# Kernel tuning notes

Measured on AMD Instinct MI355X. Metric: run time of the kernel, lower is better.

Reference implementation:

```python
import jax, jax.numpy as jnp
import numpy as np

B, D, LC, LQ = 64, 128, 1024, 128
NEG = -1e30


def setup_inputs() -> dict:
    key = jax.random.key(0)
    k1, k2, k3 = jax.random.split(key, 3)
    lim = float(np.sqrt(1.0 / D))
    return {
        "C": jax.random.normal(k1, (B, D, LC), dtype=jnp.float32),
        "Q": jax.random.normal(k2, (B, D, LQ), dtype=jnp.float32),
        "cmask": jnp.ones((B, LC), dtype=jnp.float32),
        "qmask": jnp.ones((B, LQ), dtype=jnp.float32),
        "w": jax.random.uniform(k3, (3 * D,), dtype=jnp.float32, minval=-lim, maxval=lim),
    }


def reference(C, Q, cmask, qmask, w):
    # C: [B, D, Lc], Q: [B, D, Lq] -> transpose to [B, L, D] as in the torch module
    Ct = jnp.swapaxes(C, 1, 2)  # [B, Lc, D]
    Qt = jnp.swapaxes(Q, 1, 2)  # [B, Lq, D]
    d = Ct.shape[-1]
    # Trilinear decomposition of the per-step concat([Qi, C, Q*C]) . w loop:
    # S[b,c,q] = Qt[b,q] . w_q + Ct[b,c] . w_c + (Ct[b,c] * w_m) . Qt[b,q]
    w_q, w_c, w_m = w[:d], w[d:2 * d], w[2 * d:]
    s_q = Qt @ w_q                                   # [B, Lq]
    s_c = Ct @ w_c                                   # [B, Lc]
    s_m = jnp.einsum("bcd,bqd->bcq", Ct * w_m, Qt)   # [B, Lc, Lq]
    S = s_m + s_c[:, :, None] + s_q[:, None, :]      # [B, Lc, Lq]

    S1 = jax.nn.softmax(S + (1.0 - qmask)[:, None, :] * NEG, axis=2)
    S2 = jax.nn.softmax(S + (1.0 - cmask)[:, :, None] * NEG, axis=1)

    A = jnp.einsum("bcq,bqd->bcd", S1, Qt)           # [B, Lc, D]
    S12 = jnp.einsum("bcq,bkq->bck", S1, S2)         # [B, Lc, Lc]
    Bt = jnp.einsum("bck,bkd->bcd", S12, Ct)         # [B, Lc, D]

    out = jnp.concatenate([Ct, A, Ct * A, Ct * Bt], axis=2)  # [B, Lc, 4D]
    # dropout is identity in eval mode
    return jnp.swapaxes(out, 1, 2)                   # [B, 4D, Lc]
```

## Files before the change

kernel.cpp:

```cpp
#include <hip/hip_runtime.h>
#include <cstdint>
#include <cstddef>

#define B_  64
#define D_  128
#define LC_ 1024
#define LQ_ 128
#define NEGV (-1e30f)
#define NINF (-3.402823466e38f)

typedef short s16x8 __attribute__((ext_vector_type(8)));
typedef float f32x4 __attribute__((ext_vector_type(4)));

__device__ __forceinline__ unsigned short f2bf(float x) {
    union { float f; unsigned u; } v; v.f = x;
    unsigned r = v.u + 0x7fffu + ((v.u >> 16) & 1u);
    return (unsigned short)(r >> 16);
}

__global__ __launch_bounds__(256) void kT_C(const float* __restrict__ C,
                                            const float* __restrict__ w,
                                            unsigned short* __restrict__ CWt) {
    __shared__ float tile[32][33];
    int t = threadIdx.x;
    int c0 = blockIdx.x * 32, d0 = blockIdx.y * 32, b = blockIdx.z;
    int cc = t & 31, r8 = t >> 5;
#pragma unroll
    for (int i = 0; i < 4; i++) {
        int dd = r8 + 8 * i;
        tile[dd][cc] = C[((size_t)b * D_ + d0 + dd) * LC_ + c0 + cc] * w[2 * D_ + d0 + dd];
    }
    __syncthreads();
#pragma unroll
    for (int i = 0; i < 4; i++) {
        int c2 = r8 + 8 * i;
        CWt[((size_t)b * LC_ + c0 + c2) * D_ + d0 + cc] = f2bf(tile[cc][c2]);
    }
}

__global__ __launch_bounds__(256) void kT_Q(const float* __restrict__ Q,
                                            unsigned short* __restrict__ Qt) {
    __shared__ float tile[32][33];
    int t = threadIdx.x;
    int q0 = blockIdx.x * 32, d0 = blockIdx.y * 32, b = blockIdx.z;
    int qq = t & 31, r8 = t >> 5;
#pragma unroll
    for (int i = 0; i < 4; i++) {
        int dd = r8 + 8 * i;
        tile[dd][qq] = Q[((size_t)b * D_ + d0 + dd) * LQ_ + q0 + qq];
    }
    __syncthreads();
#pragma unroll
    for (int i = 0; i < 4; i++) {
        int q2 = r8 + 8 * i;
        Qt[((size_t)b * LQ_ + q0 + q2) * D_ + d0 + qq] = f2bf(tile[qq][q2]);
    }
}

__global__ __launch_bounds__(256) void k0_sq(const float* __restrict__ Q,
                                             const float* __restrict__ w,
                                             float* __restrict__ sq_g) {
    int idx = blockIdx.x * 256 + threadIdx.x;
    int b = idx >> 7, q = idx & 127;
    float s = 0.f;
    for (int d = 0; d < D_; d++) s += Q[((size_t)b * D_ + d) * LQ_ + q] * w[d];
    sq_g[idx] = s;
}

__global__ __launch_bounds__(256) void k0_sc(const float* __restrict__ C,
                                             const float* __restrict__ w,
                                             float* __restrict__ sc_g) {
    int idx = blockIdx.x * 256 + threadIdx.x;
    int b = idx >> 10, c = idx & 1023;
    float s = 0.f;
    for (int d = 0; d < D_; d++) s += C[((size_t)b * D_ + d) * LC_ + c] * w[D_ + d];
    sc_g[idx] = s;
}

__global__ __launch_bounds__(256) void kA_S(const unsigned short* __restrict__ CWt,
                                            const unsigned short* __restrict__ Qt,
                                            const float* __restrict__ sc_g,
                                            const float* __restrict__ sq_g,
                                            float* __restrict__ S_g) {
    __shared__ unsigned short Aw[128 * 136];
    __shared__ unsigned short Bq[128 * 136];
    __shared__ float sc_l[128], sq_l[128];
    int t = threadIdx.x;
    int b = blockIdx.y, c0 = blockIdx.x * 128;
    if (t < 128) {
        sc_l[t] = sc_g[b * LC_ + c0 + t];
        sq_l[t] = sq_g[b * LQ_ + t];
    }
    const uint4* gA = (const uint4*)(CWt + ((size_t)b * LC_ + c0) * D_);
    const uint4* gB = (const uint4*)(Qt + (size_t)b * LQ_ * D_);
#pragma unroll
    for (int i = 0; i < 8; i++) {
        int g = i * 256 + t;
        int row = g >> 4, col = g & 15;
        *(uint4*)&Aw[row * 136 + col * 8] = gA[g];
        *(uint4*)&Bq[row * 136 + col * 8] = gB[g];
    }
    __syncthreads();
    int w = t >> 6, l = t & 63, quad = l >> 4, lp = l & 15;
    int w32 = w * 32;
    f32x4 zero = {0.f, 0.f, 0.f, 0.f};
    f32x4 acc[2][8];
#pragma unroll
    for (int mc = 0; mc < 2; mc++)
#pragma unroll
        for (int qt = 0; qt < 8; qt++) acc[mc][qt] = zero;

#pragma unroll
    for (int ks = 0; ks < 4; ks++) {
        s16x8 a[2], bb[8];
        a[0] = *(const s16x8*)&Aw[(w32 + lp) * 136 + ks * 32 + quad * 8];
        a[1] = *(const s16x8*)&Aw[(w32 + 16 + lp) * 136 + ks * 32 + quad * 8];
#pragma unroll
        for (int qt = 0; qt < 8; qt++)
            bb[qt] = *(const s16x8*)&Bq[(qt * 16 + lp) * 136 + ks * 32 + quad * 8];
#pragma unroll
        for (int mc = 0; mc < 2; mc++)
#pragma unroll
            for (int qt = 0; qt < 8; qt++)
                acc[mc][qt] = __builtin_amdgcn_mfma_f32_16x16x32_bf16(a[mc], bb[qt], acc[mc][qt], 0, 0, 0);
    }
#pragma unroll
    for (int mc = 0; mc < 2; mc++)
#pragma unroll
        for (int i = 0; i < 4; i++) {
            int cl = w32 + mc * 16 + quad * 4 + i;
            float scv = sc_l[cl];
            size_t rb = ((size_t)b * LC_ + c0 + cl) * LQ_;
#pragma unroll
            for (int qt = 0; qt < 8; qt++) {
                int q = qt * 16 + lp;
                S_g[rb + q] = acc[mc][qt][i] + scv + sq_l[q];
            }
        }
}

__global__ __launch_bounds__(256) void krow(const float* __restrict__ S_g,
                                            const float* __restrict__ qmask,
                                            float* __restrict__ rowmax_g,
                                            float* __restrict__ rowsum_g) {
    int t = threadIdx.x, w = t >> 6, l = t & 63;
    int b = blockIdx.y;
    int r = blockIdx.x * 4 + w;
    size_t rb = ((size_t)b * LC_ + r) * LQ_;
    float v0 = S_g[rb + l] + (1.0f - qmask[b * LQ_ + l]) * NEGV;
    float v1 = S_g[rb + 64 + l] + (1.0f - qmask[b * LQ_ + 64 + l]) * NEGV;
    float m = fmaxf(v0, v1);
#pragma unroll
    for (int off = 1; off < 64; off <<= 1) m = fmaxf(m, __shfl_xor(m, off, 64));
    float s = __expf(v0 - m) + __expf(v1 - m);
#pragma unroll
    for (int off = 1; off < 64; off <<= 1) s += __shfl_xor(s, off, 64);
    if (l == 0) { rowmax_g[b * LC_ + r] = m; rowsum_g[b * LC_ + r] = s; }
}

__global__ __launch_bounds__(128) void k2a(const float* __restrict__ S_g,
                                           const float* __restrict__ cmask,
                                           float* __restrict__ pmax,
                                           float* __restrict__ psum) {
    int q = threadIdx.x;
    int b = blockIdx.y;
    int chunk = blockIdx.x;
    int cbase = chunk * 32;
    float m = NINF, s = 0.f;
    for (int cc = 0; cc < 32; cc++) {
        int c = cbase + cc;
        float v = S_g[((size_t)b * LC_ + c) * LQ_ + q] + (1.0f - cmask[b * LC_ + c]) * NEGV;
        float mn = fmaxf(m, v);
        s = s * __expf(m - mn) + __expf(v - mn);
        m = mn;
    }
    pmax[((size_t)b * 32 + chunk) * LQ_ + q] = m;
    psum[((size_t)b * 32 + chunk) * LQ_ + q] = s;
}

__global__ __launch_bounds__(128) void k2b(const float* __restrict__ pmax,
                                           const float* __restrict__ psum,
                                           float* __restrict__ colmax_g,
                                           float* __restrict__ colsum_g) {
    int q = threadIdx.x;
    int b = blockIdx.x;
    float m = NINF;
    for (int j = 0; j < 32; j++) m = fmaxf(m, pmax[((size_t)b * 32 + j) * LQ_ + q]);
    float s = 0.f;
    for (int j = 0; j < 32; j++)
        s += psum[((size_t)b * 32 + j) * LQ_ + q] * __expf(pmax[((size_t)b * 32 + j) * LQ_ + q] - m);
    colmax_g[b * LQ_ + q] = m;
    colsum_g[b * LQ_ + q] = s;
}

__global__ __launch_bounds__(256) void kB_T2(const float* __restrict__ C,
                                             const float* __restrict__ S_g,
                                             const float* __restrict__ cmask,
                                             const float* __restrict__ colmax_g,
                                             float* __restrict__ T2p) {
    __shared__ unsigned short Ca[128 * 40];
    __shared__ unsigned short Et[128 * 40];
    __shared__ float cm_l[128];
    int t = threadIdx.x;
    int b = blockIdx.y, kc = blockIdx.x;
    int cbase = kc * 256;
    if (t < 128) cm_l[t] = colmax_g[b * LQ_ + t];
    int w = t >> 6, l = t & 63, quad = l >> 4, lp = l & 15;
    int w32 = w * 32;
    f32x4 zero = {0.f, 0.f, 0.f, 0.f};
    f32x4 acc[2][8];
#pragma unroll
    for (int mc = 0; mc < 2; mc++)
#pragma unroll
        for (int qt = 0; qt < 8; qt++) acc[mc][qt] = zero;
    __syncthreads();

    for (int cb = 0; cb < 256; cb += 32) {
        {
            int d = t >> 1, half = t & 1;
            const float4* src = (const float4*)(C + ((size_t)b * D_ + d) * LC_ + cbase + cb + half * 16);
            unsigned short* dst = &Ca[d * 40 + half * 16];
#pragma unroll
            for (int j = 0; j < 4; j++) {
                float4 v = src[j];
                ushort4 o;
                o.x = f2bf(v.x); o.y = f2bf(v.y); o.z = f2bf(v.z); o.w = f2bf(v.w);
                *(ushort4*)&dst[j * 4] = o;
            }
        }
        {
            int cc = t >> 3, qb = (t & 7) * 16;
            int cg = cbase + cb + cc;
            float cmv = (1.0f - cmask[b * LC_ + cg]) * NEGV;
            const float4* src = (const float4*)(S_g + ((size_t)b * LC_ + cg) * LQ_ + qb);
#pragma unroll
            for (int j = 0; j < 4; j++) {
                float4 v = src[j];
                int q = qb + j * 4;
                Et[(q + 0) * 40 + cc] = f2bf(__expf(v.x + cmv - cm_l[q + 0]));
                Et[(q + 1) * 40 + cc] = f2bf(__expf(v.y + cmv - cm_l[q + 1]));
                Et[(q + 2) * 40 + cc] = f2bf(__expf(v.z + cmv - cm_l[q + 2]));
                Et[(q + 3) * 40 + cc] = f2bf(__expf(v.w + cmv - cm_l[q + 3]));
            }
        }
        __syncthreads();
        s16x8 a[2], bb[8];
        a[0] = *(const s16x8*)&Ca[(w32 + lp) * 40 + quad * 8];
        a[1] = *(const s16x8*)&Ca[(w32 + 16 + lp) * 40 + quad * 8];
#pragma unroll
        for (int qt = 0; qt < 8; qt++)
            bb[qt] = *(const s16x8*)&Et[(qt * 16 + lp) * 40 + quad * 8];
#pragma unroll
        for (int mc = 0; mc < 2; mc++)
#pragma unroll
            for (int qt = 0; qt < 8; qt++)
                acc[mc][qt] = __builtin_amdgcn_mfma_f32_16x16x32_bf16(a[mc], bb[qt], acc[mc][qt], 0, 0, 0);
        __syncthreads();
    }
    size_t base = (size_t)kc * ((size_t)B_ * D_ * LQ_) + (size_t)b * D_ * LQ_;
#pragma unroll
    for (int mc = 0; mc < 2; mc++)
#pragma unroll
        for (int i = 0; i < 4; i++) {
            int d = w32 + mc * 16 + quad * 4 + i;
#pragma unroll
            for (int qt = 0; qt < 8; qt++)
                T2p[base + (size_t)d * LQ_ + qt * 16 + lp] = acc[mc][qt][i];
        }
}

__global__ __launch_bounds__(256) void k3b(const float* __restrict__ T2p,
                                           const float* __restrict__ colsum_g,
                                           float* __restrict__ T2s) {
    int idx = blockIdx.x * 256 + threadIdx.x;
    const int N = B_ * D_ * LQ_;
    int b = idx >> 14, q = idx & 127;
    float s = T2p[idx] + T2p[idx + N] + T2p[idx + 2 * N] + T2p[idx + 3 * N];
    T2s[idx] = s / colsum_g[b * LQ_ + q];
}

__global__ __launch_bounds__(256) void kC_out(const float* __restrict__ C,
                                              const float* __restrict__ Q,
                                              const float* __restrict__ qmask,
                                              const float* __restrict__ S_g,
                                              const float* __restrict__ rowmax_g,
                                              const float* __restrict__ rowsum_g,
                                              const float* __restrict__ T2s,
                                              float* __restrict__ out) {
    __shared__ unsigned short S1[128 * 136];
    __shared__ unsigned short Aq[128 * 72];
    __shared__ unsigned short At[128 * 72];
    __shared__ float rm_l[128], ri_l[128], qm_l[128];
    int t = threadIdx.x;
    int b = blockIdx.y, c0 = blockIdx.x * 128;
    if (t < 128) {
        rm_l[t] = rowmax_g[b * LC_ + c0 + t];
        ri_l[t] = 1.0f / rowsum_g[b * LC_ + c0 + t];
        qm_l[t] = qmask[b * LQ_ + t];
    }
    __syncthreads();
    {
        int cc = t >> 1, qb = (t & 1) * 64;
        float rm = rm_l[cc], ri = ri_l[cc];
        const float4* src = (const float4*)(S_g + ((size_t)b * LC_ + c0 + cc) * LQ_ + qb);
        unsigned short* dst = &S1[cc * 136 + qb];
#pragma unroll
        for (int j = 0; j < 16; j++) {
            float4 v = src[j];
            int q = qb + j * 4;
            ushort4 o;
            o.x = f2bf(__expf(v.x + (1.0f - qm_l[q + 0]) * NEGV - rm) * ri);
            o.y = f2bf(__expf(v.y + (1.0f - qm_l[q + 1]) * NEGV - rm) * ri);
            o.z = f2bf(__expf(v.z + (1.0f - qm_l[q + 2]) * NEGV - rm) * ri);
            o.w = f2bf(__expf(v.w + (1.0f - qm_l[q + 3]) * NEGV - rm) * ri);
            *(ushort4*)&dst[j * 4] = o;
        }
    }
    int w = t >> 6, l = t & 63, quad = l >> 4, lp = l & 15;
    int w32 = w * 32;
    f32x4 zero = {0.f, 0.f, 0.f, 0.f};
    f32x4 accA[2][8], accB[2][8];
#pragma unroll
    for (int mc = 0; mc < 2; mc++)
#pragma unroll
        for (int nt = 0; nt < 8; nt++) { accA[mc][nt] = zero; accB[mc][nt] = zero; }

    for (int kq = 0; kq < 2; kq++) {
        __syncthreads();
        {
            int d = t >> 1, qoff = (t & 1) * 32;
            const float4* sq4 = (const float4*)(Q + ((size_t)b * D_ + d) * LQ_ + kq * 64 + qoff);
            const float4* st4 = (const float4*)(T2s + ((size_t)b * D_ + d) * LQ_ + kq * 64 + qoff);
            unsigned short* dq = &Aq[d * 72 + qoff];
            unsigned short* dt = &At[d * 72 + qoff];
#pragma unroll
            for (int j = 0; j < 8; j++) {
                float4 v = sq4[j];
                ushort4 o;
                o.x = f2bf(v.x); o.y = f2bf(v.y); o.z = f2bf(v.z); o.w = f2bf(v.w);
                *(ushort4*)&dq[j * 4] = o;
                float4 u = st4[j];
                ushort4 p;
                p.x = f2bf(u.x); p.y = f2bf(u.y); p.z = f2bf(u.z); p.w = f2bf(u.w);
                *(ushort4*)&dt[j * 4] = p;
            }
        }
        __syncthreads();
#pragma unroll
        for (int ks = 0; ks < 2; ks++) {
            s16x8 aq[2], at[2], bb[8];
            aq[0] = *(const s16x8*)&Aq[(w32 + lp) * 72 + ks * 32 + quad * 8];
            aq[1] = *(const s16x8*)&Aq[(w32 + 16 + lp) * 72 + ks * 32 + quad * 8];
            at[0] = *(const s16x8*)&At[(w32 + lp) * 72 + ks * 32 + quad * 8];
            at[1] = *(const s16x8*)&At[(w32 + 16 + lp) * 72 + ks * 32 + quad * 8];
#pragma unroll
            for (int nt = 0; nt < 8; nt++)
                bb[nt] = *(const s16x8*)&S1[(nt * 16 + lp) * 136 + kq * 64 + ks * 32 + quad * 8];
#pragma unroll
            for (int mc = 0; mc < 2; mc++)
#pragma unroll
                for (int nt = 0; nt < 8; nt++) {
                    accA[mc][nt] = __builtin_amdgcn_mfma_f32_16x16x32_bf16(aq[mc], bb[nt], accA[mc][nt], 0, 0, 0);
                    accB[mc][nt] = __builtin_amdgcn_mfma_f32_16x16x32_bf16(at[mc], bb[nt], accB[mc][nt], 0, 0, 0);
                }
        }
    }
    const size_t DL = (size_t)D_ * LC_;
#pragma unroll
    for (int mc = 0; mc < 2; mc++)
#pragma unroll
        for (int i = 0; i < 4; i++) {
            int d = w32 + mc * 16 + quad * 4 + i;
            const float* Crow = C + ((size_t)b * D_ + d) * LC_ + c0;
            size_t ob = ((size_t)b * 4 * D_ + d) * LC_ + c0;
#pragma unroll
            for (int nt = 0; nt < 8; nt++) {
                int c = nt * 16 + lp;
                float cv = Crow[c];
                float a = accA[mc][nt][i];
                float bt = accB[mc][nt][i];
                out[ob + c] = cv;
                out[ob + DL + c] = a;
                out[ob + 2 * DL + c] = cv * a;
                out[ob + 3 * DL + c] = cv * bt;
            }
        }
}

extern "C" void kernel_launch(void* const* d_in, const int* in_sizes, int n_in,
                              void* d_out, int out_size, void* d_ws, size_t ws_size,
                              hipStream_t stream) {
    const float* C     = (const float*)d_in[0];
    const float* Q     = (const float*)d_in[1];
    const float* cmask = (const float*)d_in[2];
    const float* qmask = (const float*)d_in[3];
    const float* w     = (const float*)d_in[4];
    float* out = (float*)d_out;

    float* ws = (float*)d_ws;
    float* S_g      = ws;
    float* rowmax_g = S_g + (size_t)B_ * LC_ * LQ_;
    float* rowsum_g = rowmax_g + (size_t)B_ * LC_;
    float* pmax     = rowsum_g + (size_t)B_ * LC_;
    float* psum     = pmax + (size_t)B_ * 32 * LQ_;
    float* colmax_g = psum + (size_t)B_ * 32 * LQ_;
    float* colsum_g = colmax_g + (size_t)B_ * LQ_;
    float* sq_g     = colsum_g + (size_t)B_ * LQ_;
    float* sc_g     = sq_g + (size_t)B_ * LQ_;
    float* T2p      = sc_g + (size_t)B_ * LC_;
    float* T2s      = T2p + (size_t)4 * B_ * D_ * LQ_;
    unsigned short* CWt = (unsigned short*)(T2s + (size_t)B_ * D_ * LQ_);
    unsigned short* Qt  = CWt + (size_t)B_ * LC_ * D_;

    kT_C<<<dim3(LC_ / 32, D_ / 32, B_), 256, 0, stream>>>(C, w, CWt);
    kT_Q<<<dim3(LQ_ / 32, D_ / 32, B_), 256, 0, stream>>>(Q, Qt);
    k0_sq<<<dim3(B_ * LQ_ / 256), 256, 0, stream>>>(Q, w, sq_g);
    k0_sc<<<dim3(B_ * LC_ / 256), 256, 0, stream>>>(C, w, sc_g);
    kA_S<<<dim3(LC_ / 128, B_), 256, 0, stream>>>(CWt, Qt, sc_g, sq_g, S_g);
    krow<<<dim3(LC_ / 4, B_), 256, 0, stream>>>(S_g, qmask, rowmax_g, rowsum_g);
    k2a<<<dim3(32, B_), 128, 0, stream>>>(S_g, cmask, pmax, psum);
    k2b<<<dim3(B_), 128, 0, stream>>>(pmax, psum, colmax_g, colsum_g);
    kB_T2<<<dim3(4, B_), 256, 0, stream>>>(C, S_g, cmask, colmax_g, T2p);
    k3b<<<dim3(B_ * D_ * LQ_ / 256), 256, 0, stream>>>(T2p, colsum_g, T2s);
    kC_out<<<dim3(LC_ / 128, B_), 256, 0, stream>>>(C, Q, qmask, S_g, rowmax_g,
                                                    rowsum_g, T2s, out);
}
```

Baseline: 265.8 us.

## Fuse softmax statistics into score GEMM and store bf16 probabilities instead of fp32 scores

The score kernel now computes the row softmax and the per-chunk column max and sum in registers. It writes bf16 S1 probabilities and a per-row factor instead of the full fp32 S matrix. The transpose kernels also produce the s_c/s_q dot products and bf16 copies of C and Q, so the separate reduction kernels and repeated fp32-to-bf16 conversions go away. The main cost removed is the fp32 S round trip through global memory and several extra launches. S2 is rebuilt algebraically from S1 with row and column scale factors, which risks overflow or precision loss because it relies on exp of large maxima, and the MFMA operands are now read straight from global memory without LDS staging.

```diff
diff --git a/kernel.cpp b/kernel.cpp
--- a/kernel.cpp
+++ b/kernel.cpp
@@ -17,92 +17,140 @@
     unsigned r = v.u + 0x7fffu + ((v.u >> 16) & 1u);
     return (unsigned short)(r >> 16);
 }
+__device__ __forceinline__ float bf2f(unsigned short x) {
+    union { unsigned u; float f; } v; v.u = ((unsigned)x) << 16;
+    return v.f;
+}
 
 __global__ __launch_bounds__(256) void kT_C(const float* __restrict__ C,
                                             const float* __restrict__ w,
-                                            unsigned short* __restrict__ CWt) {
+                                            unsigned short* __restrict__ CWt,
+                                            unsigned short* __restrict__ Cb,
+                                            float* __restrict__ sc_g) {
     __shared__ float tile[32][33];
+    __shared__ float wc_l[128], wm_l[128];
+    __shared__ float red[8][32];
     int t = threadIdx.x;
-    int c0 = blockIdx.x * 32, d0 = blockIdx.y * 32, b = blockIdx.z;
-    int cc = t & 31, r8 = t >> 5;
-#pragma unroll
-    for (int i = 0; i < 4; i++) {
-        int dd = r8 + 8 * i;
-        tile[dd][cc] = C[((size_t)b * D_ + d0 + dd) * LC_ + c0 + cc] * w[2 * D_ + d0 + dd];
-    }
-    __syncthreads();
-#pragma unroll
-    for (int i = 0; i < 4; i++) {
-        int c2 = r8 + 8 * i;
-        CWt[((size_t)b * LC_ + c0 + c2) * D_ + d0 + cc] = f2bf(tile[cc][c2]);
+    int b = blockIdx.y, c0 = blockIdx.x * 32;
+    if (t < 128) { wc_l[t] = w[D_ + t]; wm_l[t] = w[2 * D_ + t]; }
+    __syncthreads();
+    float scp = 0.f;
+    int cc = t & 31, db = t >> 5;
+    for (int ch = 0; ch < 4; ch++) {
+#pragma unroll
+        for (int i = 0; i < 4; i++) {
+            int dl = db * 4 + i;
+            float v = C[((size_t)(b * D_ + ch * 32 + dl)) * LC_ + c0 + cc];
+            tile[dl][cc] = v;
+            scp += v * wc_l[ch * 32 + dl];
+        }
+        __syncthreads();
+        {
+            int c2 = t >> 3, ds = (t & 7) * 4;
+            ushort4 o;
+            o.x = f2bf(tile[ds + 0][c2] * wm_l[ch * 32 + ds + 0]);
+            o.y = f2bf(tile[ds + 1][c2] * wm_l[ch * 32 + ds + 1]);
+            o.z = f2bf(tile[ds + 2][c2] * wm_l[ch * 32 + ds + 2]);
+            o.w = f2bf(tile[ds + 3][c2] * wm_l[ch * 32 + ds + 3]);
+            *(ushort4*)&CWt[((size_t)(b * LC_ + c0 + c2)) * D_ + ch * 32 + ds] = o;
+        }
+        {
+            int d2 = t >> 3, cs = (t & 7) * 4;
+            ushort4 o;
+            o.x = f2bf(tile[d2][cs + 0]);
+            o.y = f2bf(tile[d2][cs + 1]);
+            o.z = f2bf(tile[d2][cs + 2]);
+            o.w = f2bf(tile[d2][cs + 3]);
+            *(ushort4*)&Cb[((size_t)(b * D_ + ch * 32 + d2)) * LC_ + c0 + cs] = o;
+        }
+        __syncthreads();
+    }
+    red[db][cc] = scp;
+    __syncthreads();
+    if (t < 32) {
+        float s = 0.f;
+#pragma unroll
+        for (int j = 0; j < 8; j++) s += red[j][t];
+        sc_g[b * LC_ + c0 + t] = s;
     }
 }
 
 __global__ __launch_bounds__(256) void kT_Q(const float* __restrict__ Q,
-                                            unsigned short* __restrict__ Qt) {
+                                            const float* __restrict__ w,
+                                            unsigned short* __restrict__ Qt,
+                                            unsigned short* __restrict__ Qb,
+                                            float* __restrict__ sq_g) {
     __shared__ float tile[32][33];
+    __shared__ float wq_l[128];
+    __shared__ float red[8][32];
     int t = threadIdx.x;
-    int q0 = blockIdx.x * 32, d0 = blockIdx.y * 32, b = blockIdx.z;
-    int qq = t & 31, r8 = t >> 5;
-#pragma unroll
-    for (int i = 0; i < 4; i++) {
-        int dd = r8 + 8 * i;
-        tile[dd][qq] = Q[((size_t)b * D_ + d0 + dd) * LQ_ + q0 + qq];
-    }
-    __syncthreads();
-#pragma unroll
-    for (int i = 0; i < 4; i++) {
-        int q2 = r8 + 8 * i;
-        Qt[((size_t)b * LQ_ + q0 + q2) * D_ + d0 + qq] = f2bf(tile[qq][q2]);
-    }
-}
-
-__global__ __launch_bounds__(256) void k0_sq(const float* __restrict__ Q,
-                                             const float* __restrict__ w,
-                                             float* __restrict__ sq_g) {
-    int idx = blockIdx.x * 256 + threadIdx.x;
-    int b = idx >> 7, q = idx & 127;
-    float s = 0.f;
-    for (int d = 0; d < D_; d++) s += Q[((size_t)b * D_ + d) * LQ_ + q] * w[d];
-    sq_g[idx] = s;
-}
-
-__global__ __launch_bounds__(256) void k0_sc(const float* __restrict__ C,
-                                             const float* __restrict__ w,
-                                             float* __restrict__ sc_g) {
-    int idx = blockIdx.x * 256 + threadIdx.x;
-    int b = idx >> 10, c = idx & 1023;
-    float s = 0.f;
-    for (int d = 0; d < D_; d++) s += C[((size_t)b * D_ + d) * LC_ + c] * w[D_ + d];
-    sc_g[idx] = s;
+    int b = blockIdx.y, q0 = blockIdx.x * 32;
+    if (t < 128) wq_l[t] = w[t];
+    __syncthreads();
+    float sqp = 0.f;
+    int qq = t & 31, db = t >> 5;
+    for (int ch = 0; ch < 4; ch++) {
+#pragma unroll
+        for (int i = 0; i < 4; i++) {
+            int dl = db * 4 + i;
+            float v = Q[((size_t)(b * D_ + ch * 32 + dl)) * LQ_ + q0 + qq];
+            tile[dl][qq] = v;
+            sqp += v * wq_l[ch * 32 + dl];
+        }
+        __syncthreads();
+        {
+            int q2 = t >> 3, ds = (t & 7) * 4;
+            ushort4 o;
+            o.x = f2bf(tile[ds + 0][q2]);
+            o.y = f2bf(tile[ds + 1][q2]);
+            o.z = f2bf(tile[ds + 2][q2]);
+            o.w = f2bf(tile[ds + 3][q2]);
+            *(ushort4*)&Qt[((size_t)(b * LQ_ + q0 + q2)) * D_ + ch * 32 + ds] = o;
+        }
+        {
+            int d2 = t >> 3, qs = (t & 7) * 4;
+            ushort4 o;
+            o.x = f2bf(tile[d2][qs + 0]);
+            o.y = f2bf(tile[d2][qs + 1]);
+            o.z = f2bf(tile[d2][qs + 2]);
+            o.w = f2bf(tile[d2][qs + 3]);
+            *(ushort4*)&Qb[((size_t)(b * D_ + ch * 32 + d2)) * LQ_ + q0 + qs] = o;
+        }
+        __syncthreads();
+    }
+    red[db][qq] = sqp;
+    __syncthreads();
+    if (t < 32) {
+        float s = 0.f;
+#pragma unroll
+        for (int j = 0; j < 8; j++) s += red[j][t];
+        sq_g[b * LQ_ + q0 + t] = s;
+    }
 }
 
 __global__ __launch_bounds__(256) void kA_S(const unsigned short* __restrict__ CWt,
                                             const unsigned short* __restrict__ Qt,
                                             const float* __restrict__ sc_g,
                                             const float* __restrict__ sq_g,
-                                            float* __restrict__ S_g) {
-    __shared__ unsigned short Aw[128 * 136];
-    __shared__ unsigned short Bq[128 * 136];
-    __shared__ float sc_l[128], sq_l[128];
+                                            const float* __restrict__ cmask,
+                                            const float* __restrict__ qmask,
+                                            unsigned short* __restrict__ S1b,
+                                            float* __restrict__ g_g,
+                                            float* __restrict__ pmax_g,
+                                            float* __restrict__ psum_g) {
+    __shared__ unsigned short S1t[128 * 136];
+    __shared__ float sc_l[128], sq_l[128], cmv_l[128], qmv_l[128];
     int t = threadIdx.x;
     int b = blockIdx.y, c0 = blockIdx.x * 128;
     if (t < 128) {
         sc_l[t] = sc_g[b * LC_ + c0 + t];
         sq_l[t] = sq_g[b * LQ_ + t];
-    }
-    const uint4* gA = (const uint4*)(CWt + ((size_t)b * LC_ + c0) * D_);
-    const uint4* gB = (const uint4*)(Qt + (size_t)b * LQ_ * D_);
-#pragma unroll
-    for (int i = 0; i < 8; i++) {
-        int g = i * 256 + t;
-        int row = g >> 4, col = g & 15;
-        *(uint4*)&Aw[row * 136 + col * 8] = gA[g];
-        *(uint4*)&Bq[row * 136 + col * 8] = gB[g];
-    }
-    __syncthreads();
-    int w = t >> 6, l = t & 63, quad = l >> 4, lp = l & 15;
-    int w32 = w * 32;
+        cmv_l[t] = (1.0f - cmask[b * LC_ + c0 + t]) * NEGV;
+        qmv_l[t] = (1.0f - qmask[b * LQ_ + t]) * NEGV;
+    }
+    __syncthreads();
+    int wv = t >> 6, l = t & 63, quad = l >> 4, lp = l & 15;
+    int w32 = wv * 32;
     f32x4 zero = {0.f, 0.f, 0.f, 0.f};
     f32x4 acc[2][8];
 #pragma unroll
@@ -113,11 +161,11 @@
 #pragma unroll
     for (int ks = 0; ks < 4; ks++) {
         s16x8 a[2], bb[8];
-        a[0] = *(const s16x8*)&Aw[(w32 + lp) * 136 + ks * 32 + quad * 8];
-        a[1] = *(const s16x8*)&Aw[(w32 + 16 + lp) * 136 + ks * 32 + quad * 8];
+        a[0] = *(const s16x8*)&CWt[((size_t)(b * LC_ + c0 + w32 + lp)) * D_ + ks * 32 + quad * 8];
+        a[1] = *(const s16x8*)&CWt[((size_t)(b * LC_ + c0 + w32 + 16 + lp)) * D_ + ks * 32 + quad * 8];
 #pragma unroll
         for (int qt = 0; qt < 8; qt++)
-            bb[qt] = *(const s16x8*)&Bq[(qt * 16 + lp) * 136 + ks * 32 + quad * 8];
+            bb[qt] = *(const s16x8*)&Qt[((size_t)(b * LQ_ + qt * 16 + lp)) * D_ + ks * 32 + quad * 8];
 #pragma unroll
         for (int mc = 0; mc < 2; mc++)
 #pragma unroll
@@ -127,197 +175,180 @@
 #pragma unroll
     for (int mc = 0; mc < 2; mc++)
 #pragma unroll
+        for (int qt = 0; qt < 8; qt++)
+#pragma unroll
+            for (int i = 0; i < 4; i++)
+                acc[mc][qt][i] += sc_l[w32 + mc * 16 + quad * 4 + i] + sq_l[qt * 16 + lp];
+
+    float qmv_r[8];
+#pragma unroll
+    for (int qt = 0; qt < 8; qt++) qmv_r[qt] = qmv_l[qt * 16 + lp];
+
+    float rm_r[2][4], ri_r[2][4];
+#pragma unroll
+    for (int mc = 0; mc < 2; mc++)
+#pragma unroll
         for (int i = 0; i < 4; i++) {
-            int cl = w32 + mc * 16 + quad * 4 + i;
-            float scv = sc_l[cl];
-            size_t rb = ((size_t)b * LC_ + c0 + cl) * LQ_;
-#pragma unroll
-            for (int qt = 0; qt < 8; qt++) {
-                int q = qt * 16 + lp;
-                S_g[rb + q] = acc[mc][qt][i] + scv + sq_l[q];
+            float m = NINF;
+#pragma unroll
+            for (int qt = 0; qt < 8; qt++) m = fmaxf(m, acc[mc][qt][i] + qmv_r[qt]);
+#pragma unroll
+            for (int off = 1; off < 16; off <<= 1) m = fmaxf(m, __shfl_xor(m, off, 64));
+            float s = 0.f;
+#pragma unroll
+            for (int qt = 0; qt < 8; qt++) s += __expf(acc[mc][qt][i] + qmv_r[qt] - m);
+#pragma unroll
+            for (int off = 1; off < 16; off <<= 1) s += __shfl_xor(s, off, 64);
+            rm_r[mc][i] = m;
+            ri_r[mc][i] = 1.0f / s;
+            int row = w32 + mc * 16 + quad * 4 + i;
+            if (lp == 0) g_g[b * LC_ + c0 + row] = s * __expf(m + cmv_l[row]);
+        }
+
+    float cmv_r[2][4];
+#pragma unroll
+    for (int mc = 0; mc < 2; mc++)
+#pragma unroll
+        for (int i = 0; i < 4; i++) cmv_r[mc][i] = cmv_l[w32 + mc * 16 + quad * 4 + i];
+    int chunk = blockIdx.x * 4 + wv;
+#pragma unroll
+    for (int qt = 0; qt < 8; qt++) {
+        float cm = NINF;
+#pragma unroll
+        for (int mc = 0; mc < 2; mc++)
+#pragma unroll
+            for (int i = 0; i < 4; i++) cm = fmaxf(cm, acc[mc][qt][i] + cmv_r[mc][i]);
+        cm = fmaxf(cm, __shfl_xor(cm, 16, 64));
+        cm = fmaxf(cm, __shfl_xor(cm, 32, 64));
+        float cs = 0.f;
+#pragma unroll
+        for (int mc = 0; mc < 2; mc++)
+#pragma unroll
+            for (int i = 0; i < 4; i++) cs += __expf(acc[mc][qt][i] + cmv_r[mc][i] - cm);
+        cs += __shfl_xor(cs, 16, 64);
+        cs += __shfl_xor(cs, 32, 64);
+        if (l < 16) {
+            pmax_g[((size_t)(b * 32 + chunk)) * LQ_ + qt * 16 + lp] = cm;
+            psum_g[((size_t)(b * 32 + chunk)) * LQ_ + qt * 16 + lp] = cs;
+        }
+    }
+
+#pragma unroll
+    for (int mc = 0; mc < 2; mc++)
+#pragma unroll
+        for (int qt = 0; qt < 8; qt++)
+#pragma unroll
+            for (int i = 0; i < 4; i++) {
+                int row = w32 + mc * 16 + quad * 4 + i;
+                float s1 = __expf(acc[mc][qt][i] + qmv_r[qt] - rm_r[mc][i]) * ri_r[mc][i];
+                S1t[row * 136 + qt * 16 + lp] = f2bf(s1);
             }
-        }
-}
-
-__global__ __launch_bounds__(256) void krow(const float* __restrict__ S_g,
-                                            const float* __restrict__ qmask,
-                                            float* __restrict__ rowmax_g,
-                                            float* __restrict__ rowsum_g) {
-    int t = threadIdx.x, w = t >> 6, l = t & 63;
-    int b = blockIdx.y;
-    int r = blockIdx.x * 4 + w;
-    size_t rb = ((size_t)b * LC_ + r) * LQ_;
-    float v0 = S_g[rb + l] + (1.0f - qmask[b * LQ_ + l]) * NEGV;
-    float v1 = S_g[rb + 64 + l] + (1.0f - qmask[b * LQ_ + 64 + l]) * NEGV;
-    float m = fmaxf(v0, v1);
-#pragma unroll
-    for (int off = 1; off < 64; off <<= 1) m = fmaxf(m, __shfl_xor(m, off, 64));
-    float s = __expf(v0 - m) + __expf(v1 - m);
-#pragma unroll
-    for (int off = 1; off < 64; off <<= 1) s += __shfl_xor(s, off, 64);
-    if (l == 0) { rowmax_g[b * LC_ + r] = m; rowsum_g[b * LC_ + r] = s; }
-}
-
-__global__ __launch_bounds__(128) void k2a(const float* __restrict__ S_g,
-                                           const float* __restrict__ cmask,
-                                           float* __restrict__ pmax,
-                                           float* __restrict__ psum) {
-    int q = threadIdx.x;
-    int b = blockIdx.y;
-    int chunk = blockIdx.x;
-    int cbase = chunk * 32;
-    float m = NINF, s = 0.f;
-    for (int cc = 0; cc < 32; cc++) {
-        int c = cbase + cc;
-        float v = S_g[((size_t)b * LC_ + c) * LQ_ + q] + (1.0f - cmask[b * LC_ + c]) * NEGV;
-        float mn = fmaxf(m, v);
-        s = s * __expf(m - mn) + __expf(v - mn);
-        m = mn;
-    }
-    pmax[((size_t)b * 32 + chunk) * LQ_ + q] = m;
-    psum[((size_t)b * 32 + chunk) * LQ_ + q] = s;
+    __syncthreads();
+    {
+        int row = t >> 1, qh = (t & 1) * 64;
+        const uint4* src = (const uint4*)&S1t[row * 136 + qh];
+        uint4* dst = (uint4*)&S1b[((size_t)(b * LC_ + c0 + row)) * LQ_ + qh];
+#pragma unroll
+        for (int j = 0; j < 8; j++) dst[j] = src[j];
+    }
 }
 
 __global__ __launch_bounds__(128) void k2b(const float* __restrict__ pmax,
                                            const float* __restrict__ psum,
-                                           float* __restrict__ colmax_g,
-                                           float* __restrict__ colsum_g) {
-    int q = threadIdx.x;
-    int b = blockIdx.x;
+                                           float* __restrict__ hq_g,
+                                           float* __restrict__ ci_g) {
+    int q = threadIdx.x, b = blockIdx.x;
     float m = NINF;
-    for (int j = 0; j < 32; j++) m = fmaxf(m, pmax[((size_t)b * 32 + j) * LQ_ + q]);
+    for (int j = 0; j < 32; j++) m = fmaxf(m, pmax[((size_t)(b * 32 + j)) * LQ_ + q]);
     float s = 0.f;
     for (int j = 0; j < 32; j++)
-        s += psum[((size_t)b * 32 + j) * LQ_ + q] * __expf(pmax[((size_t)b * 32 + j) * LQ_ + q] - m);
-    colmax_g[b * LQ_ + q] = m;
-    colsum_g[b * LQ_ + q] = s;
-}
-
-__global__ __launch_bounds__(256) void kB_T2(const float* __restrict__ C,
-                                             const float* __restrict__ S_g,
-                                             const float* __restrict__ cmask,
-                                             const float* __restrict__ colmax_g,
+        s += psum[((size_t)(b * 32 + j)) * LQ_ + q] * __expf(pmax[((size_t)(b * 32 + j)) * LQ_ + q] - m);
+    hq_g[b * LQ_ + q] = __expf(-m);
+    ci_g[b * LQ_ + q] = 1.0f / s;
+}
+
+__global__ __launch_bounds__(256) void kB_T2(const unsigned short* __restrict__ Cb,
+                                             const unsigned short* __restrict__ S1b,
+                                             const float* __restrict__ g_g,
+                                             const float* __restrict__ hq_g,
                                              float* __restrict__ T2p) {
-    __shared__ unsigned short Ca[128 * 40];
-    __shared__ unsigned short Et[128 * 40];
-    __shared__ float cm_l[128];
+    __shared__ unsigned short Ew[64 * 72];
+    __shared__ float h_l[64];
     int t = threadIdx.x;
-    int b = blockIdx.y, kc = blockIdx.x;
-    int cbase = kc * 256;
-    if (t < 128) cm_l[t] = colmax_g[b * LQ_ + t];
-    int w = t >> 6, l = t & 63, quad = l >> 4, lp = l & 15;
-    int w32 = w * 32;
+    int b = blockIdx.y;
+    int kc = blockIdx.x >> 1, nq = blockIdx.x & 1;
+    int q0 = nq * 64, cbase = kc * 256;
+    if (t < 64) h_l[t] = hq_g[b * LQ_ + q0 + t];
+    int wv = t >> 6, l = t & 63, quad = l >> 4, lp = l & 15;
+    int w32 = wv * 32;
     f32x4 zero = {0.f, 0.f, 0.f, 0.f};
-    f32x4 acc[2][8];
-#pragma unroll
-    for (int mc = 0; mc < 2; mc++)
-#pragma unroll
-        for (int qt = 0; qt < 8; qt++) acc[mc][qt] = zero;
-    __syncthreads();
-
-    for (int cb = 0; cb < 256; cb += 32) {
-        {
-            int d = t >> 1, half = t & 1;
-            const float4* src = (const float4*)(C + ((size_t)b * D_ + d) * LC_ + cbase + cb + half * 16);
-            unsigned short* dst = &Ca[d * 40 + half * 16];
-#pragma unroll
-            for (int j = 0; j < 4; j++) {
-                float4 v = src[j];
-                ushort4 o;
-                o.x = f2bf(v.x); o.y = f2bf(v.y); o.z = f2bf(v.z); o.w = f2bf(v.w);
-                *(ushort4*)&dst[j * 4] = o;
-            }
-        }
-        {
-            int cc = t >> 3, qb = (t & 7) * 16;
-            int cg = cbase + cb + cc;
-            float cmv = (1.0f - cmask[b * LC_ + cg]) * NEGV;
-            const float4* src = (const float4*)(S_g + ((size_t)b * LC_ + cg) * LQ_ + qb);
-#pragma unroll
-            for (int j = 0; j < 4; j++) {
-                float4 v = src[j];
-                int q = qb + j * 4;
-                Et[(q + 0) * 40 + cc] = f2bf(__expf(v.x + cmv - cm_l[q + 0]));
-                Et[(q + 1) * 40 + cc] = f2bf(__expf(v.y + cmv - cm_l[q + 1]));
-                Et[(q + 2) * 40 + cc] = f2bf(__expf(v.z + cmv - cm_l[q + 2]));
-                Et[(q + 3) * 40 + cc] = f2bf(__expf(v.w + cmv - cm_l[q + 3]));
-            }
-        }
-        __syncthreads();
-        s16x8 a[2], bb[8];
-        a[0] = *(const s16x8*)&Ca[(w32 + lp) * 40 + quad * 8];
-        a[1] = *(const s16x8*)&Ca[(w32 + 16 + lp) * 40 + quad * 8];
-#pragma unroll
-        for (int qt = 0; qt < 8; qt++)
-            bb[qt] = *(const s16x8*)&Et[(qt * 16 + lp) * 40 + quad * 8];
-#pragma unroll
-        for (int mc = 0; mc < 2; mc++)
-#pragma unroll
-            for (int qt = 0; qt < 8; qt++)
-                acc[mc][qt] = __builtin_amdgcn_mfma_f32_16x16x32_bf16(a[mc], bb[qt], acc[mc][qt], 0, 0, 0);
-        __syncthreads();
-    }
-    size_t base = (size_t)kc * ((size_t)B_ * D_ * LQ_) + (size_t)b * D_ * LQ_;
+    f32x4 acc[2][4];
+#pragma unroll
+    for (int mc = 0; mc < 2; mc++)
+#pragma unroll
+        for (int nt = 0; nt < 4; nt++) acc[mc][nt] = zero;
+    __syncthreads();
+
+    for (int sub = 0; sub < 4; sub++) {
+        int csub = cbase + sub * 64;
+#pragma unroll
+        for (int r = 0; r < 2; r++) {
+            int cr = (t >> 3) + 32 * r;
+            int qof = (t & 7) * 8;
+            float gv = g_g[b * LC_ + csub + cr];
+            uint4 v = *(const uint4*)&S1b[((size_t)(b * LC_ + csub + cr)) * LQ_ + q0 + qof];
+            const unsigned short* pu = (const unsigned short*)&v;
+#pragma unroll
+            for (int j = 0; j < 8; j++)
+                Ew[(qof + j) * 72 + cr] = f2bf(bf2f(pu[j]) * gv * h_l[qof + j]);
+        }
+        __syncthreads();
+#pragma unroll
+        for (int ks = 0; ks < 2; ks++) {
+            s16x8 a[2], bb[4];
+            a[0] = *(const s16x8*)&Cb[((size_t)(b * D_ + w32 + lp)) * LC_ + csub + ks * 32 + quad * 8];
+            a[1] = *(const s16x8*)&Cb[((size_t)(b * D_ + w32 + 16 + lp)) * LC_ + csub + ks * 32 + quad * 8];
+#pragma unroll
+            for (int nt = 0; nt < 4; nt++)
+                bb[nt] = *(const s16x8*)&Ew[(nt * 16 + lp) * 72 + ks * 32 + quad * 8];
+#pragma unroll
+            for (int mc = 0; mc < 2; mc++)
+#pragma unroll
+                for (int nt = 0; nt < 4; nt++)
+                    acc[mc][nt] = __builtin_amdgcn_mfma_f32_16x16x32_bf16(a[mc], bb[nt], acc[mc][nt], 0, 0, 0);
+        }
+        __syncthreads();
+    }
 #pragma unroll
     for (int mc = 0; mc < 2; mc++)
 #pragma unroll
         for (int i = 0; i < 4; i++) {
             int d = w32 + mc * 16 + quad * 4 + i;
 #pragma unroll
-            for (int qt = 0; qt < 8; qt++)
-                T2p[base + (size_t)d * LQ_ + qt * 16 + lp] = acc[mc][qt][i];
+            for (int nt = 0; nt < 4; nt++)
+                T2p[(((size_t)kc * B_ + b) * D_ + d) * LQ_ + q0 + nt * 16 + lp] = acc[mc][nt][i];
         }
 }
 
 __global__ __launch_bounds__(256) void k3b(const float* __restrict__ T2p,
-                                           const float* __restrict__ colsum_g,
-                                           float* __restrict__ T2s) {
+                                           const float* __restrict__ ci_g,
+                                           unsigned short* __restrict__ T2b) {
     int idx = blockIdx.x * 256 + threadIdx.x;
-    const int N = B_ * D_ * LQ_;
+    const size_t N = (size_t)B_ * D_ * LQ_;
     int b = idx >> 14, q = idx & 127;
     float s = T2p[idx] + T2p[idx + N] + T2p[idx + 2 * N] + T2p[idx + 3 * N];
-    T2s[idx] = s / colsum_g[b * LQ_ + q];
+    T2b[idx] = f2bf(s * ci_g[b * LQ_ + q]);
 }
 
 __global__ __launch_bounds__(256) void kC_out(const float* __restrict__ C,
-                                              const float* __restrict__ Q,
-                                              const float* __restrict__ qmask,
-                                              const float* __restrict__ S_g,
-                                              const float* __restrict__ rowmax_g,
-                                              const float* __restrict__ rowsum_g,
-                                              const float* __restrict__ T2s,
+                                              const unsigned short* __restrict__ Qb,
+                                              const unsigned short* __restrict__ T2b,
+                                              const unsigned short* __restrict__ S1b,
                                               float* __restrict__ out) {
-    __shared__ unsigned short S1[128 * 136];
-    __shared__ unsigned short Aq[128 * 72];
-    __shared__ unsigned short At[128 * 72];
-    __shared__ float rm_l[128], ri_l[128], qm_l[128];
     int t = threadIdx.x;
     int b = blockIdx.y, c0 = blockIdx.x * 128;
-    if (t < 128) {
-        rm_l[t] = rowmax_g[b * LC_ + c0 + t];
-        ri_l[t] = 1.0f / rowsum_g[b * LC_ + c0 + t];
-        qm_l[t] = qmask[b * LQ_ + t];
-    }
-    __syncthreads();
-    {
-        int cc = t >> 1, qb = (t & 1) * 64;
-        float rm = rm_l[cc], ri = ri_l[cc];
-        const float4* src = (const float4*)(S_g + ((size_t)b * LC_ + c0 + cc) * LQ_ + qb);
-        unsigned short* dst = &S1[cc * 136 + qb];
-#pragma unroll
-        for (int j = 0; j < 16; j++) {
-            float4 v = src[j];
-            int q = qb + j * 4;
-            ushort4 o;
-            o.x = f2bf(__expf(v.x + (1.0f - qm_l[q + 0]) * NEGV - rm) * ri);
-            o.y = f2bf(__expf(v.y + (1.0f - qm_l[q + 1]) * NEGV - rm) * ri);
-            o.z = f2bf(__expf(v.z + (1.0f - qm_l[q + 2]) * NEGV - rm) * ri);
-            o.w = f2bf(__expf(v.w + (1.0f - qm_l[q + 3]) * NEGV - rm) * ri);
-            *(ushort4*)&dst[j * 4] = o;
-        }
-    }
-    int w = t >> 6, l = t & 63, quad = l >> 4, lp = l & 15;
-    int w32 = w * 32;
+    int wv = t >> 6, l = t & 63, quad = l >> 4, lp = l & 15;
+    int w32 = wv * 32;
     f32x4 zero = {0.f, 0.f, 0.f, 0.f};
     f32x4 accA[2][8], accB[2][8];
 #pragma unroll
@@ -325,45 +356,23 @@
 #pragma unroll
         for (int nt = 0; nt < 8; nt++) { accA[mc][nt] = zero; accB[mc][nt] = zero; }
 
-    for (int kq = 0; kq < 2; kq++) {
-        __syncthreads();
-        {
-            int d = t >> 1, qoff = (t & 1) * 32;
-            const float4* sq4 = (const float4*)(Q + ((size_t)b * D_ + d) * LQ_ + kq * 64 + qoff);
-            const float4* st4 = (const float4*)(T2s + ((size_t)b * D_ + d) * LQ_ + kq * 64 + qoff);
-            unsigned short* dq = &Aq[d * 72 + qoff];
-            unsigned short* dt = &At[d * 72 + qoff];
-#pragma unroll
-            for (int j = 0; j < 8; j++) {
-                float4 v = sq4[j];
-                ushort4 o;
-                o.x = f2bf(v.x); o.y = f2bf(v.y); o.z = f2bf(v.z); o.w = f2bf(v.w);
-                *(ushort4*)&dq[j * 4] = o;
-                float4 u = st4[j];
-                ushort4 p;
-                p.x = f2bf(u.x); p.y = f2bf(u.y); p.z = f2bf(u.z); p.w = f2bf(u.w);
-                *(ushort4*)&dt[j * 4] = p;
+#pragma unroll
+    for (int ks = 0; ks < 4; ks++) {
+        s16x8 aq[2], at[2], bb[8];
+        aq[0] = *(const s16x8*)&Qb[((size_t)(b * D_ + w32 + lp)) * LQ_ + ks * 32 + quad * 8];
+        aq[1] = *(const s16x8*)&Qb[((size_t)(b * D_ + w32 + 16 + lp)) * LQ_ + ks * 32 + quad * 8];
+        at[0] = *(const s16x8*)&T2b[((size_t)(b * D_ + w32 + lp)) * LQ_ + ks * 32 + quad * 8];
+        at[1] = *(const s16x8*)&T2b[((size_t)(b * D_ + w32 + 16 + lp)) * LQ_ + ks * 32 + quad * 8];
+#pragma unroll
+        for (int nt = 0; nt < 8; nt++)
+            bb[nt] = *(const s16x8*)&S1b[((size_t)(b * LC_ + c0 + nt * 16 + lp)) * LQ_ + ks * 32 + quad * 8];
+#pragma unroll
+        for (int mc = 0; mc < 2; mc++)
+#pragma unroll
+            for (int nt = 0; nt < 8; nt++) {
+                accA[mc][nt] = __builtin_amdgcn_mfma_f32_16x16x32_bf16(aq[mc], bb[nt], accA[mc][nt], 0, 0, 0);
+                accB[mc][nt] = __builtin_amdgcn_mfma_f32_16x16x32_bf16(at[mc], bb[nt], accB[mc][nt], 0, 0, 0);
             }
-        }
-        __syncthreads();
-#pragma unroll
-        for (int ks = 0; ks < 2; ks++) {
-            s16x8 aq[2], at[2], bb[8];
-            aq[0] = *(const s16x8*)&Aq[(w32 + lp) * 72 + ks * 32 + quad * 8];
-            aq[1] = *(const s16x8*)&Aq[(w32 + 16 + lp) * 72 + ks * 32 + quad * 8];
-            at[0] = *(const s16x8*)&At[(w32 + lp) * 72 + ks * 32 + quad * 8];
-            at[1] = *(const s16x8*)&At[(w32 + 16 + lp) * 72 + ks * 32 + quad * 8];
-#pragma unroll
-            for (int nt = 0; nt < 8; nt++)
-                bb[nt] = *(const s16x8*)&S1[(nt * 16 + lp) * 136 + kq * 64 + ks * 32 + quad * 8];
-#pragma unroll
-            for (int mc = 0; mc < 2; mc++)
-#pragma unroll
-                for (int nt = 0; nt < 8; nt++) {
-                    accA[mc][nt] = __builtin_amdgcn_mfma_f32_16x16x32_bf16(aq[mc], bb[nt], accA[mc][nt], 0, 0, 0);
-                    accB[mc][nt] = __builtin_amdgcn_mfma_f32_16x16x32_bf16(at[mc], bb[nt], accB[mc][nt], 0, 0, 0);
-                }
-        }
     }
     const size_t DL = (size_t)D_ * LC_;
 #pragma unroll
@@ -371,8 +380,8 @@
 #pragma unroll
         for (int i = 0; i < 4; i++) {
             int d = w32 + mc * 16 + quad * 4 + i;
-            const float* Crow = C + ((size_t)b * D_ + d) * LC_ + c0;
-            size_t ob = ((size_t)b * 4 * D_ + d) * LC_ + c0;
+            const float* Crow = C + ((size_t)(b * D_ + d)) * LC_ + c0;
+            size_t ob = ((size_t)(b * 4 * D_ + d)) * LC_ + c0;
 #pragma unroll
             for (int nt = 0; nt < 8; nt++) {
                 int c = nt * 16 + lp;
@@ -397,31 +406,29 @@
     const float* w     = (const float*)d_in[4];
     float* out = (float*)d_out;
 
-    float* ws = (float*)d_ws;
-    float* S_g      = ws;
-    float* rowmax_g = S_g + (size_t)B_ * LC_ * LQ_;
-    float* rowsum_g = rowmax_g + (size_t)B_ * LC_;
-    float* pmax     = rowsum_g + (size_t)B_ * LC_;
-    float* psum     = pmax + (size_t)B_ * 32 * LQ_;
-    float* colmax_g = psum + (size_t)B_ * 32 * LQ_;
-    float* colsum_g = colmax_g + (size_t)B_ * LQ_;
-    float* sq_g     = colsum_g + (size_t)B_ * LQ_;
-    float* sc_g     = sq_g + (size_t)B_ * LQ_;
-    float* T2p      = sc_g + (size_t)B_ * LC_;
-    float* T2s      = T2p + (size_t)4 * B_ * D_ * LQ_;
-    unsigned short* CWt = (unsigned short*)(T2s + (size_t)B_ * D_ * LQ_);
-    unsigned short* Qt  = CWt + (size_t)B_ * LC_ * D_;
-
-    kT_C<<<dim3(LC_ / 32, D_ / 32, B_), 256, 0, stream>>>(C, w, CWt);
-    kT_Q<<<dim3(LQ_ / 32, D_ / 32, B_), 256, 0, stream>>>(Q, Qt);
-    k0_sq<<<dim3(B_ * LQ_ / 256), 256, 0, stream>>>(Q, w, sq_g);
-    k0_sc<<<dim3(B_ * LC_ / 256), 256, 0, stream>>>(C, w, sc_g);
-    kA_S<<<dim3(LC_ / 128, B_), 256, 0, stream>>>(CWt, Qt, sc_g, sq_g, S_g);
-    krow<<<dim3(LC_ / 4, B_), 256, 0, stream>>>(S_g, qmask, rowmax_g, rowsum_g);
-    k2a<<<dim3(32, B_), 128, 0, stream>>>(S_g, cmask, pmax, psum);
-    k2b<<<dim3(B_), 128, 0, stream>>>(pmax, psum, colmax_g, colsum_g);
-    kB_T2<<<dim3(4, B_), 256, 0, stream>>>(C, S_g, cmask, colmax_g, T2p);
-    k3b<<<dim3(B_ * D_ * LQ_ / 256), 256, 0, stream>>>(T2p, colsum_g, T2s);
-    kC_out<<<dim3(LC_ / 128, B_), 256, 0, stream>>>(C, Q, qmask, S_g, rowmax_g,
-                                                    rowsum_g, T2s, out);
-}
+    unsigned short* us = (unsigned short*)d_ws;
+    unsigned short* S1b = us;
+    unsigned short* CWt = S1b + (size_t)B_ * LC_ * LQ_;
+    unsigned short* Cb  = CWt + (size_t)B_ * LC_ * D_;
+    unsigned short* Qt  = Cb  + (size_t)B_ * D_ * LC_;
+    unsigned short* Qb  = Qt  + (size_t)B_ * LQ_ * D_;
+    unsigned short* T2b = Qb  + (size_t)B_ * D_ * LQ_;
+    float* fp = (float*)(T2b + (size_t)B_ * D_ * LQ_);
+    float* T2p    = fp;
+    float* sc_g   = T2p + (size_t)4 * B_ * D_ * LQ_;
+    float* g_g    = sc_g + (size_t)B_ * LC_;
+    float* pmax_g = g_g + (size_t)B_ * LC_;
+    float* psum_g = pmax_g + (size_t)B_ * 32 * LQ_;
+    float* sq_g   = psum_g + (size_t)B_ * 32 * LQ_;
+    float* hq_g   = sq_g + (size_t)B_ * LQ_;
+    float* ci_g   = hq_g + (size_t)B_ * LQ_;
+
+    kT_C<<<dim3(LC_ / 32, B_), 256, 0, stream>>>(C, w, CWt, Cb, sc_g);
+    kT_Q<<<dim3(LQ_ / 32, B_), 256, 0, stream>>>(Q, w, Qt, Qb, sq_g);
+    kA_S<<<dim3(LC_ / 128, B_), 256, 0, stream>>>(CWt, Qt, sc_g, sq_g, cmask, qmask,
+                                                  S1b, g_g, pmax_g, psum_g);
+    k2b<<<dim3(B_), 128, 0, stream>>>(pmax_g, psum_g, hq_g, ci_g);
+    kB_T2<<<dim3(8, B_), 256, 0, stream>>>(Cb, S1b, g_g, hq_g, T2p);
+    k3b<<<dim3(B_ * D_ * LQ_ / 256), 256, 0, stream>>>(T2p, ci_g, T2b);
+    kC_out<<<dim3(LC_ / 128, B_), 256, 0, stream>>>(C, Qb, T2b, S1b, out);
+}
```

Result: faster. 254.8 us (-4.1%).
